# Kernel optimization log

Hardware: AMD Instinct MI355X
Metric: run time of the kernel (lower is better)

## Reference

```python
import jax, jax.numpy as jnp
import numpy as np

B, NSIDE, NH = 4, 64, 8
N = 12 * NSIDE * NSIDE          # HEALPix pixel count, nested ordering
CIN, CHID, COUT = 256, 512, 256
WS = 16                          # window = 4**(w+1) nested pixels, w=1
HD = CHID // NH


def _ln(x, g, b, eps=1e-5):
    m = x.mean(-1, keepdims=True)
    v = ((x - m) ** 2).mean(-1, keepdims=True)
    return (x - m) * jax.lax.rsqrt(v + eps) * g + b


def _win_attn(x, qkv_w, qkv_b, pw, pb):
    b_, n_, c = x.shape
    nw = n_ // WS
    xw = x.reshape(b_, nw, WS, c)
    qkv = xw @ qkv_w + qkv_b                      # [B, nw, ws, 3C]
    q, k, v = jnp.split(qkv, 3, axis=-1)
    def heads(t):
        return t.reshape(b_, nw, WS, NH, HD).transpose(0, 1, 3, 2, 4)
    q, k, v = heads(q), heads(k), heads(v)        # [B, nw, H, ws, hd]
    a = jax.nn.softmax(jnp.einsum('bwhqd,bwhkd->bwhqk', q, k) * (HD ** -0.5), axis=-1)
    o = jnp.einsum('bwhqk,bwhkd->bwhqd', a, v)
    o = o.transpose(0, 1, 3, 2, 4).reshape(b_, n_, c)
    return o @ pw + pb


def _heal_block(x, p, shift):
    if shift:
        x = jnp.roll(x, -WS // 2, axis=1)          # shifted-window (cyclic in nested order)
    x = x + _win_attn(_ln(x, p['ln1g'], p['ln1b']), p['qkvw'], p['qkvb'], p['pw'], p['pb'])
    h = _ln(x, p['ln2g'], p['ln2b'])
    h = jax.nn.gelu(h @ p['m1w'] + p['m1b'], approximate=False) @ p['m2w'] + p['m2b']
    x = x + h
    if shift:
        x = jnp.roll(x, WS // 2, axis=1)
    return x


def _sn_linear(h, W, b, u):
    # torch spectral_norm: one power-iteration, u/v detached, sigma = u' W v
    v = W @ u                                      # [CHID]
    v = jax.lax.stop_gradient(v / (jnp.linalg.norm(v) + 1e-12))
    u2 = v @ W                                     # [COUT]
    u2 = jax.lax.stop_gradient(u2 / (jnp.linalg.norm(u2) + 1e-12))
    sigma = v @ W @ u2
    return h @ (W / sigma) + b


def setup_inputs() -> dict:
    key = jax.random.key(0)
    ks = iter(jax.random.split(key, 64))
    def w(shape, s=0.02):
        return jax.random.normal(next(ks), shape, jnp.float32) * s
    inp = {'x': jax.random.normal(next(ks), (B, N, CIN), jnp.float32)}
    inp['ff1_w'] = w((CIN, CHID)); inp['ff1_b'] = jnp.zeros((CHID,), jnp.float32)
    for pre in ('a', 'b'):
        inp[f'{pre}_ln1g'] = jnp.ones((CHID,), jnp.float32)
        inp[f'{pre}_ln1b'] = jnp.zeros((CHID,), jnp.float32)
        inp[f'{pre}_qkvw'] = w((CHID, 3 * CHID)); inp[f'{pre}_qkvb'] = jnp.zeros((3 * CHID,), jnp.float32)
        inp[f'{pre}_pw'] = w((CHID, CHID)); inp[f'{pre}_pb'] = jnp.zeros((CHID,), jnp.float32)
        inp[f'{pre}_ln2g'] = jnp.ones((CHID,), jnp.float32)
        inp[f'{pre}_ln2b'] = jnp.zeros((CHID,), jnp.float32)
        inp[f'{pre}_m1w'] = w((CHID, 4 * CHID)); inp[f'{pre}_m1b'] = jnp.zeros((4 * CHID,), jnp.float32)
        inp[f'{pre}_m2w'] = w((4 * CHID, CHID)); inp[f'{pre}_m2b'] = jnp.zeros((CHID,), jnp.float32)
    inp['ff2_w'] = w((CHID, COUT)); inp['ff2_b'] = jnp.zeros((COUT,), jnp.float32)
    inp['ff2_u'] = jax.random.normal(next(ks), (COUT,), jnp.float32)
    return inp


def reference(x, ff1_w, ff1_b,
              a_ln1g, a_ln1b, a_qkvw, a_qkvb, a_pw, a_pb, a_ln2g, a_ln2b, a_m1w, a_m1b, a_m2w, a_m2b,
              b_ln1g, b_ln1b, b_qkvw, b_qkvb, b_pw, b_pb, b_ln2g, b_ln2b, b_m1w, b_m1b, b_m2w, b_m2b,
              ff2_w, ff2_b, ff2_u):
    pa = dict(ln1g=a_ln1g, ln1b=a_ln1b, qkvw=a_qkvw, qkvb=a_qkvb, pw=a_pw, pb=a_pb,
              ln2g=a_ln2g, ln2b=a_ln2b, m1w=a_m1w, m1b=a_m1b, m2w=a_m2w, m2b=a_m2b)
    pb_ = dict(ln1g=b_ln1g, ln1b=b_ln1b, qkvw=b_qkvw, qkvb=b_qkvb, pw=b_pw, pb=b_pb,
               ln2g=b_ln2g, ln2b=b_ln2b, m1w=b_m1w, m1b=b_m1b, m2w=b_m2w, m2b=b_m2b)
    h = jax.nn.gelu(x @ ff1_w + ff1_b, approximate=False)   # feed_forward1
    h = _heal_block(h, pa, shift=False)                     # message_passing1
    h = _heal_block(h, pb_, shift=True)                     # message_passing2
    return _sn_linear(h, ff2_w, ff2_b, ff2_u)               # spectral-norm linear
```

## Files before the change

### kernel.cpp

```cpp
#include <hip/hip_runtime.h>
#include <hip/hip_bf16.h>
#include <math.h>

typedef _Float16 f16;
typedef __attribute__((ext_vector_type(8))) _Float16 f16x8;
typedef __attribute__((ext_vector_type(4))) float f32x4;

#define DINLINE __device__ __forceinline__

DINLINE float gelu_exact(float x) {
  return 0.5f * x * (1.0f + erff(x * 0.70710678118654752f));
}
DINLINE void gload16(const void* g, void* l) {
  __builtin_amdgcn_global_load_lds((const __attribute__((address_space(1))) void*)g,
                                   (__attribute__((address_space(3))) void*)l, 16, 0, 0);
}

template <int EPI>
__global__ __launch_bounds__(512, 2) void gemm256(
    const f16* __restrict__ A, const f16* __restrict__ Bt,
    const float* __restrict__ bias, const f16* __restrict__ Cin,
    float* __restrict__ Cf, f16* __restrict__ Cb,
    const float* __restrict__ scale_ptr,
    int N, int K, int nct)
{
  __shared__ alignas(16) f16 sm[2][2][16384];

  const int nwg = (int)gridDim.x;
  const int gid = (int)blockIdx.x;
  const int q = nwg >> 3, r = nwg & 7;
  const int xcd = gid & 7, idx = gid >> 3;
  const int swz = (xcd < r ? xcd * (q + 1) : r * (q + 1) + (xcd - r) * q) + idx;
  const int rt = swz / nct, ct = swz - rt * nct;
  const int m0 = rt << 8, n0 = ct << 8;

  const int tid = (int)threadIdx.x;
  const int lane = tid & 63;
  const int wid = tid >> 6;
  const int wr = wid >> 2, wc = wid & 3;

  const int srow = tid >> 3;
  const int sslot = (tid & 7) ^ (srow & 7);
  const size_t aG0 = (size_t)(m0 + srow) * K + sslot * 8;
  const size_t bG0 = (size_t)(n0 + srow) * K + sslot * 8;
  const int sL0 = tid * 8;

  const int rsel = lane & 15, khi = lane >> 4, kx = lane & 7;
  const int swk0 = ((khi) ^ kx) << 3;
  const int swk1 = ((4 + khi) ^ kx) << 3;
  const int arow0 = wr * 128 + rsel;
  const int brow0 = wc * 64 + rsel;

  f32x4 acc[8][4] = {};
  f16x8 aF[4][2], bF0[2][2], bF1[2][2];

  const int NT = K >> 6;

#define STAGE(b, k0)                                                          \
  {                                                                           \
    _Pragma("unroll")                                                         \
    for (int j = 0; j < 4; ++j)                                               \
      gload16(A + aG0 + (size_t)j * 64 * K + (k0), &sm[b][0][j * 4096 + sL0]);\
    _Pragma("unroll")                                                         \
    for (int j = 0; j < 4; ++j)                                               \
      gload16(Bt + bG0 + (size_t)j * 64 * K + (k0), &sm[b][1][j * 4096 + sL0]);\
  }

#define LOADA(smA, MQ)                                                        \
  {                                                                           \
    _Pragma("unroll")                                                         \
    for (int i = 0; i < 4; ++i) {                                             \
      aF[i][0] = *(const f16x8*)((smA) + (arow0 + (MQ)*64 + i*16)*64 + swk0); \
      aF[i][1] = *(const f16x8*)((smA) + (arow0 + (MQ)*64 + i*16)*64 + swk1); \
    }                                                                         \
  }

#define LOADB(smB, BF, NQ)                                                    \
  {                                                                           \
    _Pragma("unroll")                                                         \
    for (int nn = 0; nn < 2; ++nn) {                                          \
      BF[nn][0] = *(const f16x8*)((smB) + (brow0 + (NQ)*32 + nn*16)*64 + swk0);\
      BF[nn][1] = *(const f16x8*)((smB) + (brow0 + (NQ)*32 + nn*16)*64 + swk1);\
    }                                                                         \
  }

#define MM(MQ, BF, NQ)                                                        \
  {                                                                           \
    __builtin_amdgcn_s_setprio(1);                                            \
    _Pragma("unroll")                                                         \
    for (int i = 0; i < 4; ++i)                                               \
      _Pragma("unroll")                                                       \
      for (int nn = 0; nn < 2; ++nn)                                          \
        _Pragma("unroll")                                                     \
        for (int kc = 0; kc < 2; ++kc)                                        \
          acc[(MQ)*4 + i][(NQ)*2 + nn] = __builtin_amdgcn_mfma_f32_16x16x32_f16( \
              aF[i][kc], BF[nn][kc], acc[(MQ)*4 + i][(NQ)*2 + nn], 0, 0, 0);  \
    __builtin_amdgcn_s_setprio(0);                                            \
  }

#define CFENCE asm volatile("" ::: "memory")

  STAGE(0, 0);
  int cur = 0;
  for (int t = 0; t < NT; ++t) {
    CFENCE;
    asm volatile("s_waitcnt vmcnt(0)" ::: "memory");
    __builtin_amdgcn_s_barrier();
    CFENCE;
    if (t + 1 < NT) {
      if (cur) STAGE(0, (t + 1) << 6) else STAGE(1, (t + 1) << 6)
    }
    const f16* smA = &sm[cur][0][0];
    const f16* smB = &sm[cur][1][0];
    LOADA(smA, 0); LOADB(smB, bF0, 0); MM(0, bF0, 0);
    __builtin_amdgcn_s_barrier(); CFENCE;
    LOADB(smB, bF1, 1); MM(0, bF1, 1);
    __builtin_amdgcn_s_barrier(); CFENCE;
    LOADA(smA, 1); MM(1, bF0, 0);
    __builtin_amdgcn_s_barrier(); CFENCE;
    MM(1, bF1, 1);
    cur ^= 1;
  }
  __builtin_amdgcn_s_barrier();
  CFENCE;

  const float scale = (EPI & 8) ? scale_ptr[0] : 1.0f;
  const int R0 = m0 + wr * 128, C0 = n0 + wc * 64;
  f16* myr = &sm[0][0][0] + wid * 8192;
#pragma unroll
  for (int m = 0; m < 8; ++m) {
#pragma unroll
    for (int n = 0; n < 4; ++n) {
      const int col = C0 + n * 16 + rsel;
      const float bb = bias ? bias[col] : 0.0f;
#pragma unroll
      for (int j = 0; j < 4; ++j) {
        const int rl = m * 16 + khi * 4 + j;
        const int row = R0 + rl;
        float v = acc[m][n][j] * scale + bb;
        if (EPI & 1) v = gelu_exact(v);
        if (EPI & 2) v += (float)Cin[(size_t)row * N + col];
        if (EPI & 4) myr[rl * 64 + n * 16 + rsel] = (f16)v;
        else         Cf[(size_t)row * N + col] = v;
      }
    }
  }
  if (EPI & 4) {
    CFENCE;
#pragma unroll
    for (int ci = 0; ci < 16; ++ci) {
      const int rl = ci * 8 + (lane >> 3);
      f16x8 v8 = *(const f16x8*)(myr + rl * 64 + (lane & 7) * 8);
      *(f16x8*)(Cb + (size_t)(R0 + rl) * N + C0 + (lane & 7) * 8) = v8;
    }
  }
#undef STAGE
#undef LOADA
#undef LOADB
#undef MM
#undef CFENCE
}

__global__ __launch_bounds__(256) void ln_f16(
    const f16* __restrict__ X, const float* __restrict__ g,
    const float* __restrict__ b, f16* __restrict__ Y)
{
  const int token = blockIdx.x * 4 + (threadIdx.x >> 6);
  const int lane = threadIdx.x & 63;
  f16x8 v = *(const f16x8*)(X + (size_t)token * 512 + lane * 8);
  float vf[8];
  float s = 0.f, s2 = 0.f;
#pragma unroll
  for (int j = 0; j < 8; ++j) { vf[j] = (float)v[j]; s += vf[j]; s2 += vf[j] * vf[j]; }
#pragma unroll
  for (int o = 32; o > 0; o >>= 1) { s += __shfl_xor(s, o, 64); s2 += __shfl_xor(s2, o, 64); }
  const float mean = s * (1.f / 512.f);
  const float inv = rsqrtf(s2 * (1.f / 512.f) - mean * mean + 1e-5f);
  const int c = lane * 8;
  f32x4 g0 = *(const f32x4*)(g + c), g1 = *(const f32x4*)(g + c + 4);
  f32x4 b0 = *(const f32x4*)(b + c), b1 = *(const f32x4*)(b + c + 4);
  f16x8 o8;
#pragma unroll
  for (int j = 0; j < 4; ++j) {
    o8[j]     = (f16)((vf[j] - mean) * inv * g0[j] + b0[j]);
    o8[4 + j] = (f16)((vf[4 + j] - mean) * inv * g1[j] + b1[j]);
  }
  *(f16x8*)(Y + (size_t)token * 512 + c) = o8;
}

__global__ __launch_bounds__(256) void cvt_f32_f16(const float* __restrict__ X,
                                                   f16* __restrict__ Y, long n8)
{
  const long i = (long)blockIdx.x * 256 + threadIdx.x;
  if (i >= n8) return;
  f32x4 v0 = *(const f32x4*)(X + i * 8), v1 = *(const f32x4*)(X + i * 8 + 4);
  f16x8 o8;
#pragma unroll
  for (int j = 0; j < 4; ++j) { o8[j] = (f16)v0[j]; o8[4 + j] = (f16)v1[j]; }
  *(f16x8*)(Y + i * 8) = o8;
}

__global__ __launch_bounds__(256) void w_tr(const float* __restrict__ W,
                                            f16* __restrict__ Wt, int K, int N)
{
  const int t = blockIdx.x * 256 + threadIdx.x;
  if (t >= K * N) return;
  const int n = t / K, k = t - n * K;
  Wt[t] = (f16)W[(size_t)k * N + n];
}

template <int SHIFT>
__global__ __launch_bounds__(256) void win_attn(const f16* __restrict__ QKV,
                                                f16* __restrict__ O)
{
  __shared__ alignas(16) f16 kv[2][16][1160];
  const int wl0 = (int)blockIdx.x * 2;
  const int tid = (int)threadIdx.x;

  for (int i = tid; i < 4096; i += 256) {
    const int win = i >> 11;
    const int rem = i & 2047;
    const int row = rem >> 7;
    const int c8 = rem & 127;
    const int src = ((wl0 + win) * 16 + row + SHIFT) % 49152;
    const int sect = c8 >> 6;
    const int hh = (c8 >> 3) & 7;
    const int dd = (c8 & 7) * 8;
    *(f16x8*)(&kv[win][row][sect * 576 + hh * 72 + dd]) =
        *(const f16x8*)(QKV + (size_t)src * 1536 + 512 + c8 * 8);
  }

  const int win = tid >> 7, h = (tid >> 4) & 7, qi = tid & 15;
  const int qtok = ((wl0 + win) * 16 + qi + SHIFT) % 49152;
  f16x8 qv[8];
#pragma unroll
  for (int c8 = 0; c8 < 8; ++c8)
    qv[c8] = *(const f16x8*)(QKV + (size_t)qtok * 1536 + h * 64 + c8 * 8);

  __syncthreads();

  float sc[16];
  float mx = -1e30f;
#pragma unroll
  for (int kj = 0; kj < 16; ++kj) {
    const f16* kr = &kv[win][kj][h * 72];
    float s = 0.f;
#pragma unroll
    for (int c8 = 0; c8 < 8; ++c8) {
      f16x8 k8 = *(const f16x8*)(kr + c8 * 8);
#pragma unroll
      for (int j = 0; j < 8; ++j) s += (float)qv[c8][j] * (float)k8[j];
    }
    s *= 0.125f;
    sc[kj] = s;
    mx = fmaxf(mx, s);
  }
  float sum = 0.f;
#pragma unroll
  for (int kj = 0; kj < 16; ++kj) { sc[kj] = expf(sc[kj] - mx); sum += sc[kj]; }
  const float inv = 1.f / sum;
  float ov[64] = {};
#pragma unroll
  for (int kj = 0; kj < 16; ++kj) {
    const float a = sc[kj] * inv;
    const f16* vr = &kv[win][kj][576 + h * 72];
#pragma unroll
    for (int c8 = 0; c8 < 8; ++c8) {
      f16x8 v8 = *(const f16x8*)(vr + c8 * 8);
#pragma unroll
      for (int j = 0; j < 8; ++j) ov[c8 * 8 + j] += a * (float)v8[j];
    }
  }
  f16* orow = O + (size_t)qtok * 512 + h * 64;
#pragma unroll
  for (int c8 = 0; c8 < 8; ++c8) {
    f16x8 t;
#pragma unroll
    for (int j = 0; j < 8; ++j) t[j] = (f16)ov[c8 * 8 + j];
    *(f16x8*)(orow + c8 * 8) = t;
  }
}

__global__ __launch_bounds__(256) void sn_sigma(const float* __restrict__ W,
                                                const float* __restrict__ u,
                                                float* __restrict__ inv_sigma)
{
  __shared__ float vsh[512];
  __shared__ float ush[256];
  __shared__ float red[256];
  const int t = (int)threadIdx.x;
  ush[t] = u[t];
  __syncthreads();
  float a0 = 0.f, a1 = 0.f;
  for (int j = 0; j < 256; ++j) {
    a0 += W[t * 256 + j] * ush[j];
    a1 += W[(t + 256) * 256 + j] * ush[j];
  }
  vsh[t] = a0; vsh[t + 256] = a1;
  red[t] = a0 * a0 + a1 * a1;
  __syncthreads();
  for (int s = 128; s > 0; s >>= 1) { if (t < s) red[t] += red[t + s]; __syncthreads(); }
  const float nv = sqrtf(red[0]) + 1e-12f;
  __syncthreads();
  const float invv = 1.f / nv;
  vsh[t] *= invv; vsh[t + 256] *= invv;
  __syncthreads();
  float u2 = 0.f;
  for (int i = 0; i < 512; ++i) u2 += vsh[i] * W[i * 256 + t];
  red[t] = u2 * u2;
  __syncthreads();
  for (int s = 128; s > 0; s >>= 1) { if (t < s) red[t] += red[t + s]; __syncthreads(); }
  const float nu = sqrtf(red[0]) + 1e-12f;
  __syncthreads();
  ush[t] = u2 / nu;
  __syncthreads();
  float d0 = 0.f, d1 = 0.f;
  for (int j = 0; j < 256; ++j) {
    d0 += W[t * 256 + j] * ush[j];
    d1 += W[(t + 256) * 256 + j] * ush[j];
  }
  red[t] = vsh[t] * d0 + vsh[t + 256] * d1;
  __syncthreads();
  for (int s = 128; s > 0; s >>= 1) { if (t < s) red[t] += red[t + s]; __syncthreads(); }
  if (t == 0) inv_sigma[0] = 1.f / red[0];
}

__global__ void fill_sentinel(float* __restrict__ out, long n, float val)
{
  const long i = (long)blockIdx.x * 256 + threadIdx.x;
  for (long k = i; k < n; k += (long)gridDim.x * 256) out[k] = val;
}

extern "C" void kernel_launch(void* const* d_in, const int* in_sizes, int n_in,
                              void* d_out, int out_size, void* d_ws, size_t ws_size,
                              hipStream_t stream)
{
  const int M = 196608;
  const int MC = 49152;
  constexpr size_t OFF_U   = 201326592ull;
  constexpr size_t OFF_OH  = 201326592ull + 150994944ull;
  constexpr size_t OFF_WT  = 402653184ull;
  constexpr size_t OFF_SIG = 415760384ull;
  constexpr size_t NEED    = OFF_SIG + 256ull;

  if (ws_size < NEED) {
    fill_sentinel<<<2048, 256, 0, stream>>>((float*)d_out, (long)out_size,
                                            (float)(ws_size >> 20));
    return;
  }

  char* ws = (char*)d_ws;
  f16* R     = (f16*)(ws);
  f16* U     = (f16*)(ws + OFF_U);
  f16* OH    = (f16*)(ws + OFF_OH);
  f16* WT    = (f16*)(ws + OFF_WT);
  float* sig = (float*)(ws + OFF_SIG);
  f16* X     = (f16*)d_out;

  const float* ff1_b = (const float*)d_in[2];
  const float* ff2_b = (const float*)d_in[28];

  f16* W_FF1 = WT;
  auto W_QKV = [&](int blk) { return WT + (blk ? 3276800 : 131072); };
  auto W_PW  = [&](int blk) { return WT + (blk ? 4063232 : 917504); };
  auto W_M1  = [&](int blk) { return WT + (blk ? 4325376 : 1179648); };
  auto W_M2  = [&](int blk) { return WT + (blk ? 5373952 : 2228224); };
  f16* W_FF2 = WT + 6422528;

  w_tr<<<512, 256, 0, stream>>>((const float*)d_in[1], W_FF1, 256, 512);
  for (int blk = 0; blk < 2; ++blk) {
    w_tr<<<3072, 256, 0, stream>>>((const float*)d_in[blk ? 17 : 5], W_QKV(blk), 512, 1536);
    w_tr<<<1024, 256, 0, stream>>>((const float*)d_in[blk ? 19 : 7], W_PW(blk), 512, 512);
    w_tr<<<4096, 256, 0, stream>>>((const float*)d_in[blk ? 23 : 11], W_M1(blk), 512, 2048);
    w_tr<<<4096, 256, 0, stream>>>((const float*)d_in[blk ? 25 : 13], W_M2(blk), 2048, 512);
  }
  w_tr<<<512, 256, 0, stream>>>((const float*)d_in[27], W_FF2, 512, 256);
  sn_sigma<<<1, 256, 0, stream>>>((const float*)d_in[27], (const float*)d_in[29], sig);

  cvt_f32_f16<<<24576, 256, 0, stream>>>((const float*)d_in[0], U, (long)M * 256 / 8);
  gemm256<5><<<1536, 512, 0, stream>>>(U, W_FF1, ff1_b, nullptr, nullptr, R, nullptr,
                                       512, 256, 2);

  for (int blk = 0; blk < 2; ++blk) {
    const float* ln1g = (const float*)d_in[blk ? 15 : 3];
    const float* ln1b = (const float*)d_in[blk ? 16 : 4];
    const float* qkvb = (const float*)d_in[blk ? 18 : 6];
    const float* pb   = (const float*)d_in[blk ? 20 : 8];
    const float* ln2g = (const float*)d_in[blk ? 21 : 9];
    const float* ln2b = (const float*)d_in[blk ? 22 : 10];
    const float* m1b  = (const float*)d_in[blk ? 24 : 12];
    const float* m2b  = (const float*)d_in[blk ? 26 : 14];

    ln_f16<<<49152, 256, 0, stream>>>(R, ln1g, ln1b, X);
    for (int mc = 0; mc < 4; ++mc) {
      const size_t ro = (size_t)mc * MC * 512;
      gemm256<4><<<1152, 512, 0, stream>>>(X + ro, W_QKV(blk), qkvb, nullptr,
                                           nullptr, U, nullptr, 1536, 512, 6);
      if (blk == 0) win_attn<0><<<1536, 256, 0, stream>>>(U, OH);
      else          win_attn<8><<<1536, 256, 0, stream>>>(U, OH);
      gemm256<6><<<384, 512, 0, stream>>>(OH, W_PW(blk), pb, R + ro,
                                          nullptr, R + ro, nullptr, 512, 512, 2);
    }
    ln_f16<<<49152, 256, 0, stream>>>(R, ln2g, ln2b, X);
    for (int mc = 0; mc < 4; ++mc) {
      const size_t ro = (size_t)mc * MC * 512;
      gemm256<5><<<1536, 512, 0, stream>>>(X + ro, W_M1(blk), m1b, nullptr,
                                           nullptr, U, nullptr, 2048, 512, 8);
      gemm256<6><<<384, 512, 0, stream>>>(U, W_M2(blk), m2b, R + ro,
                                          nullptr, R + ro, nullptr, 512, 2048, 2);
    }
  }

  gemm256<8><<<768, 512, 0, stream>>>(R, W_FF2, ff2_b, nullptr, (float*)d_out,
                                      nullptr, sig, 256, 512, 1);
}
```

Measured before the change: 5.231 ms.

## Restructure GEMM main loop into fine-grained half-tile staged pipeline

Reworks the 256x256 GEMM mainloop so shared memory is split into four 32-wide K sub-tiles per buffer. Global-to-LDS loads are issued in quarter-tile steps interleaved with each MFMA phase, and a partial vmcnt wait replaces the full drain before each tile. This aims to keep global loads in flight across compute and avoid stalling on whole-tile loads each iteration. The LDS swizzle pattern also changes to match the 32-element row layout. The cost is more barriers per tile and a hand-tuned prologue and epilogue that assume NT>=2.

```diff
diff --git a/kernel.cpp b/kernel.cpp
--- a/kernel.cpp
+++ b/kernel.cpp
@@ -15,6 +15,10 @@
   __builtin_amdgcn_global_load_lds((const __attribute__((address_space(1))) void*)g,
                                    (__attribute__((address_space(3))) void*)l, 16, 0, 0);
 }
+
+#define BAR       __builtin_amdgcn_s_barrier()
+#define WAITLGKM  asm volatile("s_waitcnt lgkmcnt(0)" ::: "memory")
+#define WAITVM(n) asm volatile("s_waitcnt vmcnt(" #n ")" ::: "memory")
 
 template <int EPI>
 __global__ __launch_bounds__(512, 2) void gemm256(
@@ -24,7 +28,7 @@
     const float* __restrict__ scale_ptr,
     int N, int K, int nct)
 {
-  __shared__ alignas(16) f16 sm[2][2][16384];
+  __shared__ alignas(16) f16 sm[2][4][8192];
 
   const int nwg = (int)gridDim.x;
   const int gid = (int)blockIdx.x;
@@ -39,94 +43,86 @@
   const int wid = tid >> 6;
   const int wr = wid >> 2, wc = wid & 3;
 
-  const int srow = tid >> 3;
-  const int sslot = (tid & 7) ^ (srow & 7);
-  const size_t aG0 = (size_t)(m0 + srow) * K + sslot * 8;
-  const size_t bG0 = (size_t)(n0 + srow) * K + sslot * 8;
-  const int sL0 = tid * 8;
-
-  const int rsel = lane & 15, khi = lane >> 4, kx = lane & 7;
-  const int swk0 = ((khi) ^ kx) << 3;
-  const int swk1 = ((4 + khi) ^ kx) << 3;
-  const int arow0 = wr * 128 + rsel;
-  const int brow0 = wc * 64 + rsel;
+  const int srow = tid >> 2;
+  const int sl = (tid & 3) ^ ((srow >> 1) & 3);
+  const size_t aG = (size_t)(m0 + srow) * K + sl * 8;
+  const size_t bG = (size_t)(n0 + srow) * K + sl * 8;
+  const int sL = tid * 8;
+
+  const int rsel = lane & 15, khi = lane >> 4;
+  const int sx = (khi ^ ((rsel >> 1) & 3)) << 3;
 
   f32x4 acc[8][4] = {};
-  f16x8 aF[4][2], bF0[2][2], bF1[2][2];
+  f16x8 aF[4], bF[4];
 
   const int NT = K >> 6;
 
-#define STAGE(b, k0)                                                          \
+#define STAGEH(h)                                                             \
+  {                                                                           \
+    const int _t = (h) >> 2, _r = (h) & 3, _b = _t & 1;                       \
+    const f16* _s = (_r & 1) ? Bt : A;                                        \
+    const size_t _g = ((_r & 1) ? bG : aG) + (size_t)_t * 64 + ((_r >> 1) << 5); \
+    gload16(_s + _g, &sm[_b][_r][sL]);                                        \
+    gload16(_s + _g + (size_t)128 * (size_t)K, &sm[_b][_r][4096 + sL]);       \
+  }
+
+#define DSRA(b, kc, mb)                                                       \
   {                                                                           \
     _Pragma("unroll")                                                         \
-    for (int j = 0; j < 4; ++j)                                               \
-      gload16(A + aG0 + (size_t)j * 64 * K + (k0), &sm[b][0][j * 4096 + sL0]);\
-    _Pragma("unroll")                                                         \
-    for (int j = 0; j < 4; ++j)                                               \
-      gload16(Bt + bG0 + (size_t)j * 64 * K + (k0), &sm[b][1][j * 4096 + sL0]);\
-  }
-
-#define LOADA(smA, MQ)                                                        \
+    for (int _i = 0; _i < 4; ++_i)                                            \
+      aF[_i] = *(const f16x8*)(&sm[b][(kc) << 1]                              \
+                  [(wr * 128 + ((mb) + _i) * 16 + rsel) * 32 + sx]);          \
+  }
+
+#define DSRB(b, kc)                                                           \
   {                                                                           \
     _Pragma("unroll")                                                         \
-    for (int i = 0; i < 4; ++i) {                                             \
-      aF[i][0] = *(const f16x8*)((smA) + (arow0 + (MQ)*64 + i*16)*64 + swk0); \
-      aF[i][1] = *(const f16x8*)((smA) + (arow0 + (MQ)*64 + i*16)*64 + swk1); \
-    }                                                                         \
-  }
-
-#define LOADB(smB, BF, NQ)                                                    \
-  {                                                                           \
-    _Pragma("unroll")                                                         \
-    for (int nn = 0; nn < 2; ++nn) {                                          \
-      BF[nn][0] = *(const f16x8*)((smB) + (brow0 + (NQ)*32 + nn*16)*64 + swk0);\
-      BF[nn][1] = *(const f16x8*)((smB) + (brow0 + (NQ)*32 + nn*16)*64 + swk1);\
-    }                                                                         \
-  }
-
-#define MM(MQ, BF, NQ)                                                        \
+    for (int _i = 0; _i < 4; ++_i)                                            \
+      bF[_i] = *(const f16x8*)(&sm[b][1 + ((kc) << 1)]                        \
+                  [(wc * 64 + _i * 16 + rsel) * 32 + sx]);                    \
+  }
+
+#define MMC(mb)                                                               \
   {                                                                           \
     __builtin_amdgcn_s_setprio(1);                                            \
     _Pragma("unroll")                                                         \
-    for (int i = 0; i < 4; ++i)                                               \
+    for (int _m = 0; _m < 4; ++_m)                                            \
       _Pragma("unroll")                                                       \
-      for (int nn = 0; nn < 2; ++nn)                                          \
-        _Pragma("unroll")                                                     \
-        for (int kc = 0; kc < 2; ++kc)                                        \
-          acc[(MQ)*4 + i][(NQ)*2 + nn] = __builtin_amdgcn_mfma_f32_16x16x32_f16( \
-              aF[i][kc], BF[nn][kc], acc[(MQ)*4 + i][(NQ)*2 + nn], 0, 0, 0);  \
+      for (int _n = 0; _n < 4; ++_n)                                          \
+        acc[(mb) + _m][_n] = __builtin_amdgcn_mfma_f32_16x16x32_f16(          \
+            aF[_m], bF[_n], acc[(mb) + _m][_n], 0, 0, 0);                     \
     __builtin_amdgcn_s_setprio(0);                                            \
   }
 
-#define CFENCE asm volatile("" ::: "memory")
-
-  STAGE(0, 0);
-  int cur = 0;
-  for (int t = 0; t < NT; ++t) {
-    CFENCE;
-    asm volatile("s_waitcnt vmcnt(0)" ::: "memory");
-    __builtin_amdgcn_s_barrier();
-    CFENCE;
-    if (t + 1 < NT) {
-      if (cur) STAGE(0, (t + 1) << 6) else STAGE(1, (t + 1) << 6)
-    }
-    const f16* smA = &sm[cur][0][0];
-    const f16* smB = &sm[cur][1][0];
-    LOADA(smA, 0); LOADB(smB, bF0, 0); MM(0, bF0, 0);
-    __builtin_amdgcn_s_barrier(); CFENCE;
-    LOADB(smB, bF1, 1); MM(0, bF1, 1);
-    __builtin_amdgcn_s_barrier(); CFENCE;
-    LOADA(smA, 1); MM(1, bF0, 0);
-    __builtin_amdgcn_s_barrier(); CFENCE;
-    MM(1, bF1, 1);
-    cur ^= 1;
-  }
-  __builtin_amdgcn_s_barrier();
-  CFENCE;
+  STAGEH(0); STAGEH(1); STAGEH(2); STAGEH(3); STAGEH(4);
+  WAITVM(6);
+  BAR;
+
+  for (int t = 0; t < NT - 2; ++t) {
+    const int b = t & 1, hb = 4 * t;
+    STAGEH(hb + 5); DSRA(b, 0, 0); DSRB(b, 0); BAR; WAITLGKM; MMC(0); WAITVM(6); BAR;
+    STAGEH(hb + 6); DSRA(b, 0, 4);             BAR; WAITLGKM; MMC(4); WAITVM(6); BAR;
+    STAGEH(hb + 7); DSRA(b, 1, 0); DSRB(b, 1); BAR; WAITLGKM; MMC(0); WAITVM(6); BAR;
+    STAGEH(hb + 8); DSRA(b, 1, 4);             BAR; WAITLGKM; MMC(4); WAITVM(6); BAR;
+  }
+  {
+    const int t = NT - 2, b = t & 1, hb = 4 * t;
+    STAGEH(hb + 5); DSRA(b, 0, 0); DSRB(b, 0); BAR; WAITLGKM; MMC(0); WAITVM(6); BAR;
+    STAGEH(hb + 6); DSRA(b, 0, 4);             BAR; WAITLGKM; MMC(4); WAITVM(6); BAR;
+    STAGEH(hb + 7); DSRA(b, 1, 0); DSRB(b, 1); BAR; WAITLGKM; MMC(0); WAITVM(6); BAR;
+                    DSRA(b, 1, 4);             BAR; WAITLGKM; MMC(4); WAITVM(4); BAR;
+  }
+  {
+    const int b = (NT - 1) & 1;
+    DSRA(b, 0, 0); DSRB(b, 0); BAR; WAITLGKM; MMC(0); WAITVM(2); BAR;
+    DSRA(b, 0, 4);             BAR; WAITLGKM; MMC(4); WAITVM(0); BAR;
+    DSRA(b, 1, 0); DSRB(b, 1); BAR; WAITLGKM; MMC(0); BAR;
+    DSRA(b, 1, 4);             BAR; WAITLGKM; MMC(4); BAR;
+  }
 
   const float scale = (EPI & 8) ? scale_ptr[0] : 1.0f;
   const int R0 = m0 + wr * 128, C0 = n0 + wc * 64;
-  f16* myr = &sm[0][0][0] + wid * 8192;
+  f16* myr = (f16*)&sm[0][0][0] + wid * 8192;
 #pragma unroll
   for (int m = 0; m < 8; ++m) {
 #pragma unroll
@@ -146,7 +142,7 @@
     }
   }
   if (EPI & 4) {
-    CFENCE;
+    asm volatile("" ::: "memory");
 #pragma unroll
     for (int ci = 0; ci < 16; ++ci) {
       const int rl = ci * 8 + (lane >> 3);
@@ -154,11 +150,10 @@
       *(f16x8*)(Cb + (size_t)(R0 + rl) * N + C0 + (lane & 7) * 8) = v8;
     }
   }
-#undef STAGE
-#undef LOADA
-#undef LOADB
-#undef MM
-#undef CFENCE
+#undef STAGEH
+#undef DSRA
+#undef DSRB
+#undef MMC
 }
 
 __global__ __launch_bounds__(256) void ln_f16(
```

New measurement: 5.219 ms. About the same (-0.2%).
